# Kernel tuning notes

Measured on AMD Instinct MI355X. Metric: run time of the kernel, lower is better.

The kernel has to match this reference:

```python
import jax, jax.numpy as jnp
import numpy as np

N_NODES = 50000
N_EDGES = 600000
EMBED_DIM = 128


def setup_inputs() -> dict:
    key = jax.random.key(0)
    k1, k2 = jax.random.split(key)
    x = jax.random.normal(k1, (N_NODES, EMBED_DIM), dtype=jnp.float32)
    edge_index = jax.random.randint(k2, (2, N_EDGES), 0, N_NODES, dtype=jnp.int64)
    bias = jnp.zeros((EMBED_DIM,), dtype=jnp.float32)
    return {"x": x, "edge_index": edge_index, "bias": bias}


def reference(x, edge_index, bias):
    # init_embedding is Identity (disable_init_embedding=True)
    init_embeds = x
    n = x.shape[0]
    # add_self_loops
    loops = jnp.arange(n, dtype=edge_index.dtype)
    row = jnp.concatenate([edge_index[0], loops])  # source nodes
    col = jnp.concatenate([edge_index[1], loops])  # destination nodes
    # degree of destination nodes
    deg = jax.ops.segment_sum(jnp.ones_like(col, dtype=x.dtype), col, num_segments=n)
    deg_inv_sqrt = jnp.where(deg > 0, jax.lax.rsqrt(jnp.maximum(deg, 1e-20)), 0.0)
    # symmetric GCN normalization per edge
    norm = deg_inv_sqrt[row] * deg_inv_sqrt[col]  # [E+N]
    # message: gather source features, scale, scatter-add into destinations
    msg = norm[:, None] * x[row]  # [E+N, D]
    out = jax.ops.segment_sum(msg, col, num_segments=n) + bias
    return (out, init_embeds)
```

## Files before the change

### kernel.cpp

```cpp
#include <hip/hip_runtime.h>

#define D 128
#define B 256
#define WMAX 64
#define SPILL_MAX 8192
#define NPART 8

typedef float vfloat4 __attribute__((ext_vector_type(4)));


__device__ __forceinline__ unsigned short f2bf(float f) {
    unsigned u = __float_as_uint(f);
    u = u + 0x7FFFu + ((u >> 16) & 1u);
    return (unsigned short)(u >> 16);
}

__device__ __forceinline__ vfloat4 bf2f4(uint2 v) {
    vfloat4 r;
    r.x = __uint_as_float(v.x << 16);
    r.y = __uint_as_float(v.x & 0xffff0000u);
    r.z = __uint_as_float(v.y << 16);
    r.w = __uint_as_float(v.y & 0xffff0000u);
    return r;
}

__global__ void k_prep(const float* __restrict__ x, float* __restrict__ out2,
                       uint2* __restrict__ xb, int* __restrict__ cursor,
                       int* __restrict__ spillCnt, int n) {
    int gid = blockIdx.x * blockDim.x + threadIdx.x;
    if (gid == 0) *spillCnt = 0;
    if (gid < n) cursor[gid] = 0;
    if (gid >= n * 32) return;
    vfloat4 xv = reinterpret_cast<const vfloat4*>(x)[gid];
    __builtin_nontemporal_store(xv, reinterpret_cast<vfloat4*>(out2) + gid);
    uint2 b;
    b.x = (unsigned)f2bf(xv.x) | ((unsigned)f2bf(xv.y) << 16);
    b.y = (unsigned)f2bf(xv.z) | ((unsigned)f2bf(xv.w) << 16);
    xb[gid] = b;
}

__global__ void k_place_ell(const int* __restrict__ row, const int* __restrict__ col,
                            int* __restrict__ cursor, int* __restrict__ ssrc,
                            int2* __restrict__ spill, int* __restrict__ spillCnt,
                            int e, int n) {
    int p  = blockIdx.x & (NPART - 1);
    int bg = blockIdx.x >> 3;
    int tg = bg * blockDim.x + threadIdx.x;
    int T  = (gridDim.x >> 3) * blockDim.x;
    int lo = (int)((long long)n * p / NPART);
    int hi = (int)((long long)n * (p + 1) / NPART);

    const int4* col4 = reinterpret_cast<const int4*>(col);
    const int4* row4 = reinterpret_cast<const int4*>(row);
    int e4 = e >> 2;

    for (int i = tg; i < e4; i += T) {
        int4 c4 = col4[i];
        int4 r4 = row4[i];
        int cs[4] = {c4.x, c4.y, c4.z, c4.w};
        int rs[4] = {r4.x, r4.y, r4.z, r4.w};
        int pos[4];
#pragma unroll
        for (int u = 0; u < 4; ++u) {
            bool keep = (cs[u] >= lo) & (cs[u] < hi);
            pos[u] = keep ? atomicAdd(&cursor[cs[u]], 1) : -1;
        }
#pragma unroll
        for (int u = 0; u < 4; ++u) {
            if (pos[u] < 0) continue;
            if (pos[u] < WMAX) {
                ssrc[cs[u] * WMAX + pos[u]] = rs[u];
            } else {
                int s = atomicAdd(spillCnt, 1);
                if (s < SPILL_MAX) spill[s] = make_int2(rs[u], cs[u]);
            }
        }
    }
    for (int i = (e4 << 2) + tg; i < e; i += T) {
        int c = col[i];
        if (c < lo || c >= hi) continue;
        int r = row[i];
        int pos = atomicAdd(&cursor[c], 1);
        if (pos < WMAX) {
            ssrc[c * WMAX + pos] = r;
        } else {
            int s = atomicAdd(spillCnt, 1);
            if (s < SPILL_MAX) spill[s] = make_int2(r, c);
        }
    }
}

__global__ void k_agg_ell(const uint2* __restrict__ xb, const float* __restrict__ bias,
                          const int* __restrict__ cursor, const int* __restrict__ ssrc,
                          const int2* __restrict__ spill, const int* __restrict__ spillCnt,
                          float* __restrict__ out, int n) {
    int p  = blockIdx.x & (NPART - 1);
    int bg = blockIdx.x >> 3;
    int lo = (int)((long long)n * p / NPART);
    int hi = (int)((long long)n * (p + 1) / NPART);
    int node = lo + bg * 8 + (threadIdx.x >> 5);
    if (node >= hi) return;
    int q = threadIdx.x & 31;

    int cnt = cursor[node];
    int m   = min(cnt, WMAX);
    const int* sp = ssrc + node * WMAX;

    vfloat4 a0 = {0.f, 0.f, 0.f, 0.f};
    vfloat4 a1 = a0, a2 = a0, a3 = a0;

    int j = 0;
    for (; j + 4 <= m; j += 4) {
        int r0 = sp[j + 0], r1 = sp[j + 1], r2 = sp[j + 2], r3 = sp[j + 3];
        uint2 v0 = xb[(size_t)r0 * 32 + q];
        uint2 v1 = xb[(size_t)r1 * 32 + q];
        uint2 v2 = xb[(size_t)r2 * 32 + q];
        uint2 v3 = xb[(size_t)r3 * 32 + q];
        float w0 = rsqrtf((float)cursor[r0] + 1.0f);
        float w1 = rsqrtf((float)cursor[r1] + 1.0f);
        float w2 = rsqrtf((float)cursor[r2] + 1.0f);
        float w3 = rsqrtf((float)cursor[r3] + 1.0f);
        a0 += w0 * bf2f4(v0);
        a1 += w1 * bf2f4(v1);
        a2 += w2 * bf2f4(v2);
        a3 += w3 * bf2f4(v3);
    }
    for (; j < m; ++j) {
        int r = sp[j];
        uint2 v = xb[(size_t)r * 32 + q];
        float w = rsqrtf((float)cursor[r] + 1.0f);
        a0 += w * bf2f4(v);
    }

    if (cnt > WMAX) {
        int sc = min(*spillCnt, SPILL_MAX);
        for (int s = 0; s < sc; ++s) {
            int2 pr = spill[s];
            if (pr.y == node) {
                float w = rsqrtf((float)cursor[pr.x] + 1.0f);
                a0 += w * bf2f4(xb[(size_t)pr.x * 32 + q]);
            }
        }
    }

    float dc = rsqrtf((float)cnt + 1.0f);
    vfloat4 xc = bf2f4(xb[(size_t)node * 32 + q]);
    vfloat4 bv = reinterpret_cast<const vfloat4*>(bias)[q];
    vfloat4 ov = bv + dc * (a0 + a1 + a2 + a3 + dc * xc);

    __builtin_nontemporal_store(ov, reinterpret_cast<vfloat4*>(out) + (size_t)node * 32 + q);
}


__global__ void k_zero(int* __restrict__ degInt, int n) {
    int i = blockIdx.x * blockDim.x + threadIdx.x;
    if (i < n) degInt[i] = 0;
}

__global__ void k_count(const int* __restrict__ col, int* __restrict__ degInt, int e) {
    int i = blockIdx.x * blockDim.x + threadIdx.x;
    if (i < e) atomicAdd(&degInt[col[i]], 1);
}

__global__ void k_scan1(const int* __restrict__ degInt, int* __restrict__ off,
                        int* __restrict__ bsum, int n) {
    __shared__ int sm[B];
    int i = blockIdx.x * B + threadIdx.x;
    int v = (i < n) ? degInt[i] : 0;
    sm[threadIdx.x] = v;
    __syncthreads();
    for (int s = 1; s < B; s <<= 1) {
        int t = (threadIdx.x >= (unsigned)s) ? sm[threadIdx.x - s] : 0;
        __syncthreads();
        sm[threadIdx.x] += t;
        __syncthreads();
    }
    if (i < n) off[i] = sm[threadIdx.x] - v;
    if (threadIdx.x == B - 1) bsum[blockIdx.x] = sm[B - 1];
}

__global__ void k_scan2(int* __restrict__ bsum, int nb) {
    __shared__ int sm[B];
    int v = (threadIdx.x < (unsigned)nb) ? bsum[threadIdx.x] : 0;
    sm[threadIdx.x] = v;
    __syncthreads();
    for (int s = 1; s < B; s <<= 1) {
        int t = (threadIdx.x >= (unsigned)s) ? sm[threadIdx.x - s] : 0;
        __syncthreads();
        sm[threadIdx.x] += t;
        __syncthreads();
    }
    if (threadIdx.x < (unsigned)nb) bsum[threadIdx.x] = sm[threadIdx.x] - v;
}

__global__ void k_scan3(int* __restrict__ off, const int* __restrict__ bsum,
                        const int* __restrict__ degInt, float* __restrict__ dis,
                        int* __restrict__ cursor, int n, int e) {
    int i = blockIdx.x * B + threadIdx.x;
    if (i < n) {
        int o = off[i] + bsum[blockIdx.x];
        off[i] = o;
        cursor[i] = o;
        dis[i] = rsqrtf((float)degInt[i] + 1.0f);
    }
    if (i == 0) off[n] = e;
}

__global__ void k_place_pairs(const int* __restrict__ row, const int* __restrict__ col,
                              const float* __restrict__ dis, int* __restrict__ cursor,
                              int2* __restrict__ pairs, int e) {
    int i = blockIdx.x * blockDim.x + threadIdx.x;
    if (i >= e) return;
    int r = row[i];
    int c = col[i];
    float w = dis[r];
    int pos = atomicAdd(&cursor[c], 1);
    pairs[pos] = make_int2(r, __float_as_int(w));
}

__global__ void k_aggregate_pairs(const float* __restrict__ x, const float* __restrict__ bias,
                                  const float* __restrict__ dis, const int* __restrict__ off,
                                  const int2* __restrict__ pairs, float* __restrict__ out,
                                  float* __restrict__ out2, int n) {
    int gid = blockIdx.x * blockDim.x + threadIdx.x;
    if (gid >= n * 32) return;
    int node = gid >> 5;
    int q    = gid & 31;
    const vfloat4* x4 = reinterpret_cast<const vfloat4*>(x);
    int j   = off[node];
    int end = off[node + 1];
    vfloat4 a0 = {0.f, 0.f, 0.f, 0.f};
    vfloat4 a1 = a0, a2 = a0, a3 = a0;
    for (; j + 4 <= end; j += 4) {
        int2 p0 = pairs[j + 0];
        int2 p1 = pairs[j + 1];
        int2 p2 = pairs[j + 2];
        int2 p3 = pairs[j + 3];
        vfloat4 v0 = x4[(size_t)p0.x * 32 + q];
        vfloat4 v1 = x4[(size_t)p1.x * 32 + q];
        vfloat4 v2 = x4[(size_t)p2.x * 32 + q];
        vfloat4 v3 = x4[(size_t)p3.x * 32 + q];
        a0 += __int_as_float(p0.y) * v0;
        a1 += __int_as_float(p1.y) * v1;
        a2 += __int_as_float(p2.y) * v2;
        a3 += __int_as_float(p3.y) * v3;
    }
    for (; j < end; ++j) {
        int2 p = pairs[j];
        a0 += __int_as_float(p.y) * x4[(size_t)p.x * 32 + q];
    }
    float dc = dis[node];
    vfloat4 xc = x4[(size_t)node * 32 + q];
    vfloat4 bv = reinterpret_cast<const vfloat4*>(bias)[q];
    vfloat4 ov = bv + dc * (a0 + a1 + a2 + a3 + dc * xc);
    __builtin_nontemporal_store(ov, reinterpret_cast<vfloat4*>(out)  + (size_t)node * 32 + q);
    __builtin_nontemporal_store(xc, reinterpret_cast<vfloat4*>(out2) + (size_t)node * 32 + q);
}


extern "C" void kernel_launch(void* const* d_in, const int* in_sizes, int n_in,
                              void* d_out, int out_size, void* d_ws, size_t ws_size,
                              hipStream_t stream) {
    const float* x    = (const float*)d_in[0];
    const int*   idx  = (const int*)d_in[1];
    const float* bias = (const float*)d_in[2];

    const int n = in_sizes[0] / D;
    const int e = in_sizes[1] / 2;

    const int* row = idx;
    const int* col = idx + e;

    float* out  = (float*)d_out;
    float* out2 = (float*)d_out + (size_t)n * D;

    const int nbN = (n + B - 1) / B;
    const int nbE = (e + B - 1) / B;
    const int aggB = (n * 32 + B - 1) / B;

    char* p0 = (char*)d_ws;
    int*  cursor  = (int*)p0;                        p0 += (size_t)n * 4;
    int*  spillCnt= (int*)p0;                        p0 += 16;
    int2* spill   = (int2*)p0;                       p0 += (size_t)SPILL_MAX * 8;
    p0 = (char*)(((uintptr_t)p0 + 15) & ~(uintptr_t)15);
    uint2* xb     = (uint2*)p0;                      p0 += (size_t)n * 32 * 8;
    int*  ssrc    = (int*)p0;                        p0 += (size_t)n * WMAX * 4;
    size_t need_ell = (size_t)(p0 - (char*)d_ws);

    if (ws_size >= need_ell) {
        const int plB = 2048;
        int maxPart = 0;
        for (int p = 0; p < NPART; ++p) {
            int lo = (int)((long long)n * p / NPART);
            int hi = (int)((long long)n * (p + 1) / NPART);
            if (hi - lo > maxPart) maxPart = hi - lo;
        }
        const int bpg = (maxPart + 7) / 8;
        const int agB = bpg * NPART;
        k_prep     <<<aggB, B, 0, stream>>>(x, out2, xb, cursor, spillCnt, n);
        k_place_ell<<<plB,  B, 0, stream>>>(row, col, cursor, ssrc, spill, spillCnt, e, n);
        k_agg_ell  <<<agB,  B, 0, stream>>>(xb, bias, cursor, ssrc, spill, spillCnt, out, n);
        return;
    }

    char* p = (char*)d_ws;
    int*   degInt = (int*)p;            p += (size_t)n * 4;
    int*   cur2   = (int*)p;            p += (size_t)n * 4;
    int*   off    = (int*)p;            p += (size_t)(n + 1) * 4;
    int*   bsum   = (int*)p;            p += 256 * 4;
    float* dis    = (float*)p;          p += (size_t)n * 4;
    p = (char*)(((uintptr_t)p + 15) & ~(uintptr_t)15);
    int2*  pairs  = (int2*)p;

    k_zero <<<nbN, B, 0, stream>>>(degInt, n);
    k_count<<<nbE, B, 0, stream>>>(col, degInt, e);
    k_scan1<<<nbN, B, 0, stream>>>(degInt, off, bsum, n);
    k_scan2<<<1,   B, 0, stream>>>(bsum, nbN);
    k_scan3<<<nbN, B, 0, stream>>>(off, bsum, degInt, dis, cur2, n, e);
    k_place_pairs<<<nbE, B, 0, stream>>>(row, col, dis, cur2, pairs, e);
    k_aggregate_pairs<<<aggB, B, 0, stream>>>(x, bias, dis, off, pairs, out, out2, n);
}
```

Measured before the change: 78.95 us.

## Pre-bucket edges by destination partition and widen aggregation loads to 16B

```diff
diff --git a/kernel.cpp b/kernel.cpp
--- a/kernel.cpp
+++ b/kernel.cpp
@@ -5,6 +5,8 @@
 #define WMAX 64
 #define SPILL_MAX 8192
 #define NPART 8
+#define CH 1024
+#define CH_SHIFT 10
 
 typedef float vfloat4 __attribute__((ext_vector_type(4)));
 
@@ -15,12 +17,12 @@
     return (unsigned short)(u >> 16);
 }
 
-__device__ __forceinline__ vfloat4 bf2f4(uint2 v) {
+__device__ __forceinline__ vfloat4 bf2f4(unsigned lo, unsigned hi) {
     vfloat4 r;
-    r.x = __uint_as_float(v.x << 16);
-    r.y = __uint_as_float(v.x & 0xffff0000u);
-    r.z = __uint_as_float(v.y << 16);
-    r.w = __uint_as_float(v.y & 0xffff0000u);
+    r.x = __uint_as_float(lo << 16);
+    r.y = __uint_as_float(lo & 0xffff0000u);
+    r.z = __uint_as_float(hi << 16);
+    r.w = __uint_as_float(hi & 0xffff0000u);
     return r;
 }
 
@@ -39,53 +41,67 @@
     xb[gid] = b;
 }
 
-__global__ void k_place_ell(const int* __restrict__ row, const int* __restrict__ col,
-                            int* __restrict__ cursor, int* __restrict__ ssrc,
-                            int2* __restrict__ spill, int* __restrict__ spillCnt,
-                            int e, int n) {
+__global__ void k_bucket(const int* __restrict__ row, const int* __restrict__ col,
+                         long long* __restrict__ bkt, int* __restrict__ cnt,
+                         int e, int n, int nBlocksA) {
+    __shared__ int lcnt[NPART];
+    int b = blockIdx.x, t = threadIdx.x;
+    if (t < NPART) lcnt[t] = 0;
+    __syncthreads();
+
+    int base = b * CH + t * 4;
+    int rs[4], cs[4];
+    bool vec_ok = ((((uintptr_t)row | (uintptr_t)col) & 15) == 0) && (base + 3 < e);
+    if (vec_ok) {
+        int4 r4 = reinterpret_cast<const int4*>(row)[base >> 2];
+        int4 c4 = reinterpret_cast<const int4*>(col)[base >> 2];
+        rs[0] = r4.x; rs[1] = r4.y; rs[2] = r4.z; rs[3] = r4.w;
+        cs[0] = c4.x; cs[1] = c4.y; cs[2] = c4.z; cs[3] = c4.w;
+    } else {
+#pragma unroll
+        for (int u = 0; u < 4; ++u) {
+            int i = base + u;
+            rs[u] = (i < e) ? row[i] : -1;
+            cs[u] = (i < e) ? col[i] : 0;
+        }
+    }
+#pragma unroll
+    for (int u = 0; u < 4; ++u) {
+        if (rs[u] < 0) continue;
+        int p = (int)((long long)cs[u] * NPART / n);
+        if (p > NPART - 1) p = NPART - 1;
+        int pos = atomicAdd(&lcnt[p], 1);
+        bkt[((size_t)p * nBlocksA + b) * CH + pos] =
+            ((long long)rs[u] << 32) | (unsigned)cs[u];
+    }
+    __syncthreads();
+    if (t < NPART) cnt[b * NPART + t] = lcnt[t];
+}
+
+__global__ void k_place2(const long long* __restrict__ bkt, const int* __restrict__ cnt,
+                         int* __restrict__ cursor, int* __restrict__ ssrc,
+                         int2* __restrict__ spill, int* __restrict__ spillCnt,
+                         int nBlocksA) {
     int p  = blockIdx.x & (NPART - 1);
     int bg = blockIdx.x >> 3;
     int tg = bg * blockDim.x + threadIdx.x;
     int T  = (gridDim.x >> 3) * blockDim.x;
-    int lo = (int)((long long)n * p / NPART);
-    int hi = (int)((long long)n * (p + 1) / NPART);
-
-    const int4* col4 = reinterpret_cast<const int4*>(col);
-    const int4* row4 = reinterpret_cast<const int4*>(row);
-    int e4 = e >> 2;
-
-    for (int i = tg; i < e4; i += T) {
-        int4 c4 = col4[i];
-        int4 r4 = row4[i];
-        int cs[4] = {c4.x, c4.y, c4.z, c4.w};
-        int rs[4] = {r4.x, r4.y, r4.z, r4.w};
-        int pos[4];
-#pragma unroll
-        for (int u = 0; u < 4; ++u) {
-            bool keep = (cs[u] >= lo) & (cs[u] < hi);
-            pos[u] = keep ? atomicAdd(&cursor[cs[u]], 1) : -1;
-        }
-#pragma unroll
-        for (int u = 0; u < 4; ++u) {
-            if (pos[u] < 0) continue;
-            if (pos[u] < WMAX) {
-                ssrc[cs[u] * WMAX + pos[u]] = rs[u];
-            } else {
-                int s = atomicAdd(spillCnt, 1);
-                if (s < SPILL_MAX) spill[s] = make_int2(rs[u], cs[u]);
-            }
-        }
-    }
-    for (int i = (e4 << 2) + tg; i < e; i += T) {
-        int c = col[i];
-        if (c < lo || c >= hi) continue;
-        int r = row[i];
-        int pos = atomicAdd(&cursor[c], 1);
+    int total = nBlocksA * CH;
+
+    for (int s = tg; s < total; s += T) {
+        int b = s >> CH_SHIFT;
+        int k = s & (CH - 1);
+        int c_ = cnt[b * NPART + p];
+        if (k >= c_) continue;
+        long long ent = __builtin_nontemporal_load(bkt + ((size_t)p * nBlocksA + b) * CH + k);
+        int r_ = (int)(ent >> 32);
+        int cdst = (int)(ent & 0xffffffffLL);
+        int pos = atomicAdd(&cursor[cdst], 1);
         if (pos < WMAX) {
-            ssrc[c * WMAX + pos] = r;
+            ssrc[cdst * WMAX + pos] = r_;
         } else {
-            int s = atomicAdd(spillCnt, 1);
-            if (s < SPILL_MAX) spill[s] = make_int2(r, c);
+            int sl = atomicAdd(spillCnt, 1);
+            if (sl < SPILL_MAX) spill[sl] = make_int2(r_, cdst);
         }
     }
 }
@@ -98,9 +114,11 @@
     int bg = blockIdx.x >> 3;
     int lo = (int)((long long)n * p / NPART);
     int hi = (int)((long long)n * (p + 1) / NPART);
-    int node = lo + bg * 8 + (threadIdx.x >> 5);
+    int node = lo + bg * 16 + (threadIdx.x >> 4);
     if (node >= hi) return;
-    int q = threadIdx.x & 31;
+    int q = threadIdx.x & 15;
+
+    const uint4* xb4 = reinterpret_cast<const uint4*>(xb);
 
     int cnt = cursor[node];
     int m   = min(cnt, WMAX);
@@ -108,28 +126,33 @@
 
     vfloat4 a0 = {0.f, 0.f, 0.f, 0.f};
     vfloat4 a1 = a0, a2 = a0, a3 = a0;
+    vfloat4 b0 = a0, b1 = a0, b2 = a0, b3 = a0;
 
     int j = 0;
     for (; j + 4 <= m; j += 4) {
-        int r0 = sp[j + 0], r1 = sp[j + 1], r2 = sp[j + 2], r3 = sp[j + 3];
-        uint2 v0 = xb[(size_t)r0 * 32 + q];
-        uint2 v1 = xb[(size_t)r1 * 32 + q];
-        uint2 v2 = xb[(size_t)r2 * 32 + q];
-        uint2 v3 = xb[(size_t)r3 * 32 + q];
+        int r0 = __builtin_nontemporal_load(sp + j + 0);
+        int r1 = __builtin_nontemporal_load(sp + j + 1);
+        int r2 = __builtin_nontemporal_load(sp + j + 2);
+        int r3 = __builtin_nontemporal_load(sp + j + 3);
+        uint4 v0 = xb4[(size_t)r0 * 16 + q];
+        uint4 v1 = xb4[(size_t)r1 * 16 + q];
+        uint4 v2 = xb4[(size_t)r2 * 16 + q];
+        uint4 v3 = xb4[(size_t)r3 * 16 + q];
         float w0 = rsqrtf((float)cursor[r0] + 1.0f);
         float w1 = rsqrtf((float)cursor[r1] + 1.0f);
         float w2 = rsqrtf((float)cursor[r2] + 1.0f);
         float w3 = rsqrtf((float)cursor[r3] + 1.0f);
-        a0 += w0 * bf2f4(v0);
-        a1 += w1 * bf2f4(v1);
-        a2 += w2 * bf2f4(v2);
-        a3 += w3 * bf2f4(v3);
+        a0 += w0 * bf2f4(v0.x, v0.y);  b0 += w0 * bf2f4(v0.z, v0.w);
+        a1 += w1 * bf2f4(v1.x, v1.y);  b1 += w1 * bf2f4(v1.z, v1.w);
+        a2 += w2 * bf2f4(v2.x, v2.y);  b2 += w2 * bf2f4(v2.z, v2.w);
+        a3 += w3 * bf2f4(v3.x, v3.y);  b3 += w3 * bf2f4(v3.z, v3.w);
     }
     for (; j < m; ++j) {
-        int r = sp[j];
-        uint2 v = xb[(size_t)r * 32 + q];
+        int r = __builtin_nontemporal_load(sp + j);
+        uint4 v = xb4[(size_t)r * 16 + q];
         float w = rsqrtf((float)cursor[r] + 1.0f);
-        a0 += w * bf2f4(v);
+        a0 += w * bf2f4(v.x, v.y);
+        b0 += w * bf2f4(v.z, v.w);
     }
 
     if (cnt > WMAX) {
@@ -138,17 +161,26 @@
             int2 pr = spill[s];
             if (pr.y == node) {
                 float w = rsqrtf((float)cursor[pr.x] + 1.0f);
-                a0 += w * bf2f4(xb[(size_t)pr.x * 32 + q]);
+                uint4 v = xb4[(size_t)pr.x * 16 + q];
+                a0 += w * bf2f4(v.x, v.y);
+                b0 += w * bf2f4(v.z, v.w);
             }
         }
     }
 
     float dc = rsqrtf((float)cnt + 1.0f);
-    vfloat4 xc = bf2f4(xb[(size_t)node * 32 + q]);
-    vfloat4 bv = reinterpret_cast<const vfloat4*>(bias)[q];
-    vfloat4 ov = bv + dc * (a0 + a1 + a2 + a3 + dc * xc);
-
-    __builtin_nontemporal_store(ov, reinterpret_cast<vfloat4*>(out) + (size_t)node * 32 + q);
+    uint4 xc = xb4[(size_t)node * 16 + q];
+    vfloat4 xcl = bf2f4(xc.x, xc.y);
+    vfloat4 xch = bf2f4(xc.z, xc.w);
+    const vfloat4* bias4 = reinterpret_cast<const vfloat4*>(bias);
+    vfloat4 bvl = bias4[q * 2];
+    vfloat4 bvh = bias4[q * 2 + 1];
+    vfloat4 ovl = bvl + dc * (a0 + a1 + a2 + a3 + dc * xcl);
+    vfloat4 ovh = bvh + dc * (b0 + b1 + b2 + b3 + dc * xch);
+
+    vfloat4* out4 = reinterpret_cast<vfloat4*>(out);
+    __builtin_nontemporal_store(ovl, out4 + (size_t)node * 32 + q * 2);
+    __builtin_nontemporal_store(ovh, out4 + (size_t)node * 32 + q * 2 + 1);
 }
 
 
@@ -276,7 +308,8 @@
 
     const int nbN = (n + B - 1) / B;
     const int nbE = (e + B - 1) / B;
-    const int aggB = (n * 32 + B - 1) / B;
+    const int prepB = (n * 32 + B - 1) / B;
+    const int nBlocksA = (e + CH - 1) / CH;
 
     char* p0 = (char*)d_ws;
     int*  cursor  = (int*)p0;                        p0 += (size_t)n * 4;
@@ -285,6 +318,9 @@
     p0 = (char*)(((uintptr_t)p0 + 15) & ~(uintptr_t)15);
     uint2* xb     = (uint2*)p0;                      p0 += (size_t)n * 32 * 8;
     int*  ssrc    = (int*)p0;                        p0 += (size_t)n * WMAX * 4;
+    p0 = (char*)(((uintptr_t)p0 + 15) & ~(uintptr_t)15);
+    long long* bkt = (long long*)p0;                 p0 += (size_t)NPART * nBlocksA * CH * 8;
+    int*  cnt     = (int*)p0;                        p0 += (size_t)nBlocksA * NPART * 4;
     size_t need_ell = (size_t)(p0 - (char*)d_ws);
 
     if (ws_size >= need_ell) {
@@ -295,11 +331,12 @@
             int hi = (int)((long long)n * (p + 1) / NPART);
             if (hi - lo > maxPart) maxPart = hi - lo;
         }
-        const int bpg = (maxPart + 7) / 8;
+        const int bpg = (maxPart + 15) / 16;
         const int agB = bpg * NPART;
-        k_prep     <<<aggB, B, 0, stream>>>(x, out2, xb, cursor, spillCnt, n);
-        k_place_ell<<<plB,  B, 0, stream>>>(row, col, cursor, ssrc, spill, spillCnt, e, n);
-        k_agg_ell  <<<agB,  B, 0, stream>>>(xb, bias, cursor, ssrc, spill, spillCnt, out, n);
+        k_prep  <<<prepB,    B, 0, stream>>>(x, out2, xb, cursor, spillCnt, n);
+        k_bucket<<<nBlocksA, B, 0, stream>>>(row, col, bkt, cnt, e, n, nBlocksA);
+        k_place2<<<plB,      B, 0, stream>>>(bkt, cnt, cursor, ssrc, spill, spillCnt, nBlocksA);
+        k_agg_ell<<<agB,     B, 0, stream>>>(xb, bias, cursor, ssrc, spill, spillCnt, out, n);
         return;
     }
 
@@ -312,6 +349,7 @@
     p = (char*)(((uintptr_t)p + 15) & ~(uintptr_t)15);
     int2*  pairs  = (int2*)p;
 
+    const int aggB = (n * 32 + B - 1) / B;
     k_zero <<<nbN, B, 0, stream>>>(degInt, n);
     k_count<<<nbE, B, 0, stream>>>(col, degInt, e);
     k_scan1<<<nbN, B, 0, stream>>>(degInt, off, bsum, n);
```

Result: slower. 96.55 us (+22.3%).
